# Kernel tuning notes

Hardware: AMD Instinct MI355X
Metric: run time of the kernel (lower is better)

Reference implementation:

```python
import jax, jax.numpy as jnp
import numpy as np

B, S, DIN, DOUT = 2, 4096, 4096, 11008

def setup_inputs() -> dict:
    key = jax.random.key(0)
    k1, k2, k3 = jax.random.split(key, 3)
    x = jax.random.normal(k1, (B, S, DIN), dtype=jnp.float32)
    # kaiming-uniform-ish full-precision weight
    bound_w = 1.0 / np.sqrt(DIN)
    weight = jax.random.uniform(k2, (DOUT, DIN), dtype=jnp.float32, minval=-bound_w, maxval=bound_w)
    bias = jax.random.uniform(k3, (DOUT,), dtype=jnp.float32, minval=-bound_w, maxval=bound_w)
    return {"x": x, "weight": weight, "bias": bias}

def reference(x, weight, bias):
    # Binarize weight to {-1, 0, +1} via sign (matches torch.sign), scale by mean |w| (detached)
    binary_w = jnp.sign(weight)                                  # [DOUT, DIN]
    scale = jax.lax.stop_gradient(jnp.mean(jnp.abs(weight)))    # scalar
    w_q = binary_w * scale
    # F.linear: x @ w_q.T + bias
    out = jnp.einsum('bsi,oi->bso', x, w_q) + bias               # [B, S, DOUT]
    return out
```

## Files before the change

kernel.cpp:

```cpp
#include <hip/hip_runtime.h>

#define MDIM 8192
#define KDIM 4096
#define NDIM 11008

#define NBLK_W 1024

typedef float f32x4 __attribute__((ext_vector_type(4)));
typedef int   i32x4 __attribute__((ext_vector_type(4)));
typedef char  c4    __attribute__((ext_vector_type(4)));

#define GAS __attribute__((address_space(1)))
#define LAS __attribute__((address_space(3)))

__global__ __launch_bounds__(256) void k_convert_w(const float* __restrict__ w,
                                                   char* __restrict__ wq,
                                                   float* __restrict__ partials) {
  const int n4 = (NDIM * KDIM) / 4;
  const int stride = gridDim.x * blockDim.x;
  float s = 0.f;
  for (int i = blockIdx.x * blockDim.x + threadIdx.x; i < n4; i += stride) {
    f32x4 v = ((const f32x4*)w)[i];
    s += fabsf(v.x) + fabsf(v.y) + fabsf(v.z) + fabsf(v.w);
    c4 q;
    q.x = v.x > 0.f ? 1 : (v.x < 0.f ? -1 : 0);
    q.y = v.y > 0.f ? 1 : (v.y < 0.f ? -1 : 0);
    q.z = v.z > 0.f ? 1 : (v.z < 0.f ? -1 : 0);
    q.w = v.w > 0.f ? 1 : (v.w < 0.f ? -1 : 0);
    ((c4*)wq)[i] = q;
  }
  #pragma unroll
  for (int off = 32; off > 0; off >>= 1) s += __shfl_down(s, off, 64);
  __shared__ float red[4];
  if ((threadIdx.x & 63) == 0) red[threadIdx.x >> 6] = s;
  __syncthreads();
  if (threadIdx.x == 0) partials[blockIdx.x] = red[0] + red[1] + red[2] + red[3];
}

__global__ __launch_bounds__(256) void k_scale(const float* __restrict__ partials,
                                               float* __restrict__ scale) {
  float s = 0.f;
  for (int i = threadIdx.x; i < NBLK_W; i += 256) s += partials[i];
  #pragma unroll
  for (int off = 32; off > 0; off >>= 1) s += __shfl_down(s, off, 64);
  __shared__ float red[4];
  if ((threadIdx.x & 63) == 0) red[threadIdx.x >> 6] = s;
  __syncthreads();
  if (threadIdx.x == 0)
    *scale = (red[0] + red[1] + red[2] + red[3]) / (float)((size_t)NDIM * KDIM);
}

__global__ __launch_bounds__(256) void k_convert_x(const float* __restrict__ x,
                                                   char* __restrict__ xq,
                                                   float* __restrict__ sx) {
  const int row = blockIdx.x;
  const float* xr = x + (size_t)row * KDIM;
  const int t = (int)threadIdx.x;
  f32x4 v[4];
  float mx = 0.f;
  #pragma unroll
  for (int j = 0; j < 4; ++j) {
    v[j] = *(const f32x4*)(xr + j * 1024 + t * 4);
    mx = fmaxf(mx, fmaxf(fmaxf(fabsf(v[j].x), fabsf(v[j].y)),
                         fmaxf(fabsf(v[j].z), fabsf(v[j].w))));
  }
  #pragma unroll
  for (int off = 32; off > 0; off >>= 1) mx = fmaxf(mx, __shfl_xor(mx, off, 64));
  __shared__ float red[4];
  __shared__ float bmax;
  if ((t & 63) == 0) red[t >> 6] = mx;
  __syncthreads();
  if (t == 0) {
    float m2 = fmaxf(fmaxf(red[0], red[1]), fmaxf(red[2], red[3]));
    m2 = fmaxf(m2, 1e-20f);
    bmax = m2;
    sx[row] = m2 * (1.f / 127.f);
  }
  __syncthreads();
  const float r = 127.f / bmax;
  #pragma unroll
  for (int j = 0; j < 4; ++j) {
    int a = __float2int_rn(v[j].x * r), b = __float2int_rn(v[j].y * r);
    int c = __float2int_rn(v[j].z * r), d = __float2int_rn(v[j].w * r);
    a = a > 127 ? 127 : (a < -127 ? -127 : a);
    b = b > 127 ? 127 : (b < -127 ? -127 : b);
    c = c > 127 ? 127 : (c < -127 ? -127 : c);
    d = d > 127 ? 127 : (d < -127 ? -127 : d);
    c4 q; q.x = (char)a; q.y = (char)b; q.z = (char)c; q.w = (char)d;
    *(c4*)(xq + (size_t)row * KDIM + j * 1024 + t * 4) = q;
  }
}


#define BAR()  __builtin_amdgcn_s_barrier()
#define SB0()  __builtin_amdgcn_sched_barrier(0)
#define PRIO1() __builtin_amdgcn_s_setprio(1)
#define PRIO0() __builtin_amdgcn_s_setprio(0)
#define VM(N)  asm volatile("s_waitcnt vmcnt(" #N ")" ::: "memory")

#define STAGE(GP, GROWB, LDSBASE, KT) do {                                            \
  const char* _s = (GP) + (size_t)((GROWB) + srow) * KDIM + (KT)*64 + scol;           \
  char* _d = lds + (LDSBASE) + tid*16;                                                \
  __builtin_amdgcn_global_load_lds((const GAS unsigned int*)_s,                       \
                                   (LAS unsigned int*)_d, 16, 0, 0);                  \
} while (0)

#define LOAD_B2(DST, BUF, NH)                                                         \
  _Pragma("unroll") for (int ni = 0; ni < 2; ++ni)                                    \
    DST[ni] = *(const i32x4*)&lds[(BUF)*24576 + 8192 + bWOff + (NH)*2048 + ni*1024    \
                                  + rowoff + rcol];

#define LOAD_A2(DST, BUF, MH)                                                         \
  _Pragma("unroll") for (int mi = 0; mi < 2; ++mi)                                    \
    DST[mi] = *(const i32x4*)&lds[(BUF)*24576 + aWOff + (MH)*2048 + mi*1024           \
                                  + rowoff + rcol];

#define MFMA4(AF, MB, BQ, NB)                                                         \
  _Pragma("unroll") for (int mi = 0; mi < 2; ++mi)                                    \
  _Pragma("unroll") for (int ni = 0; ni < 2; ++ni)                                    \
    acc[(MB)+mi][(NB)+ni] = __builtin_amdgcn_mfma_i32_16x16x64_i8(                    \
        AF[mi], BQ[ni], acc[(MB)+mi][(NB)+ni], 0, 0, 0);

__global__ __launch_bounds__(512, 4) void k_gemm256(const char* __restrict__ A,
                                                    const char* __restrict__ B,
                                                    const float* __restrict__ bias,
                                                    const float* __restrict__ sx,
                                                    const float* __restrict__ scale_p,
                                                    float* __restrict__ C) {
  extern __shared__ char lds[];

  const int nTn = NDIM / 256;
  const int nwg = (MDIM / 128) * nTn;
  int wg = (int)blockIdx.x;
  wg = (wg & 7) * (nwg / 8) + (wg >> 3);
  const int band = wg / (nTn * 8);
  const int rem  = wg % (nTn * 8);
  const int tn   = rem >> 3;
  const int tm   = band * 8 + (rem & 7);

  const int tid  = (int)threadIdx.x;
  const int lane = tid & 63;
  const int wave = tid >> 6;
  const int wm   = wave >> 2;
  const int wn   = wave & 3;
  const int l15  = lane & 15;

  const int rowoff = l15 * 64;
  const int rcol = ((lane >> 4) << 4) ^ (((l15 >> 1) & 3) << 4);
  const int srow = tid >> 2;
  const int scol = ((tid & 3) << 4) ^ (((tid >> 3) & 3) << 4);

  const int aWOff = wm * 4096;
  const int bWOff = wn * 4096;
  const int aRow = tm * 128;
  const int bRow = tn * 256;

  i32x4 acc[4][4];
  #pragma unroll
  for (int i = 0; i < 4; ++i)
    #pragma unroll
    for (int j = 0; j < 4; ++j) acc[i][j] = i32x4{0, 0, 0, 0};

  i32x4 af[2], bq01[2], bq23[2];

  STAGE(A, aRow,        0,     0);
  STAGE(B, bRow,        8192,  0);
  STAGE(B, bRow + 128,  16384, 0);
  STAGE(A, aRow,        24576, 1);
  VM(0);
  SB0();
  BAR();
  LOAD_A2(af, 0, 0); LOAD_B2(bq01, 0, 0);

  #pragma unroll 1
  for (int i = 0; i < 32; ++i) {
    const int kA = 2 * i + 1;
    const int kB = (2 * i + 2 > 63) ? 63 : 2 * i + 2;
    const int kC = (2 * i + 3 > 63) ? 63 : 2 * i + 3;
    PRIO1(); MFMA4(af, 0, bq01, 0); PRIO0(); SB0();
    LOAD_B2(bq23, 0, 1);
    STAGE(B, bRow,       32768, kA);
    BAR();
    PRIO1(); MFMA4(af, 0, bq23, 2); PRIO0(); SB0();
    LOAD_A2(af, 0, 1);
    STAGE(B, bRow + 128, 40960, kA);
    BAR();
    PRIO1(); MFMA4(af, 2, bq01, 0); PRIO0(); SB0();
    VM(0); SB0();
    BAR();
    PRIO1(); MFMA4(af, 2, bq23, 2); PRIO0(); SB0();
    LOAD_A2(af, 1, 0); LOAD_B2(bq01, 1, 0);
    STAGE(A, aRow,       0,     kB);
    BAR();
    PRIO1(); MFMA4(af, 0, bq01, 0); PRIO0(); SB0();
    LOAD_B2(bq23, 1, 1);
    STAGE(B, bRow,       8192,  kB);
    BAR();
    PRIO1(); MFMA4(af, 0, bq23, 2); PRIO0(); SB0();
    LOAD_A2(af, 1, 1);
    STAGE(B, bRow + 128, 16384, kB);
    BAR();
    PRIO1(); MFMA4(af, 2, bq01, 0); PRIO0(); SB0();
    VM(0); SB0();
    BAR();
    PRIO1(); MFMA4(af, 2, bq23, 2); PRIO0(); SB0();
    LOAD_A2(af, 0, 0); LOAD_B2(bq01, 0, 0);
    STAGE(A, aRow,       24576, kC);
    BAR();
  }

  VM(0);

  const float sc = *scale_p;
  float bv[4];
  #pragma unroll
  for (int ni = 0; ni < 4; ++ni) bv[ni] = bias[tn * 256 + wn * 64 + ni * 16 + l15];

  #pragma unroll
  for (int mi = 0; mi < 4; ++mi) {
    #pragma unroll
    for (int r = 0; r < 4; ++r) {
      const int m = tm * 128 + wm * 64 + mi * 16 + (lane >> 4) * 4 + r;
      const float srow_scale = sc * sx[m];
      float* crow = C + (size_t)m * NDIM + tn * 256 + wn * 64;
      #pragma unroll
      for (int ni = 0; ni < 4; ++ni)
        crow[ni * 16 + l15] = srow_scale * (float)acc[mi][ni][r] + bv[ni];
    }
  }
}

extern "C" void kernel_launch(void* const* d_in, const int* in_sizes, int n_in,
                              void* d_out, int out_size, void* d_ws, size_t ws_size,
                              hipStream_t stream) {
  const float* x = (const float*)d_in[0];
  const float* w = (const float*)d_in[1];
  const float* bias = (const float*)d_in[2];
  float* out = (float*)d_out;

  char* ws = (char*)d_ws;
  const size_t XQ_BYTES = (size_t)MDIM * KDIM;
  const size_t WQ_BYTES = (size_t)NDIM * KDIM;
  char* xq = ws;
  char* wq = ws + XQ_BYTES;
  float* sx = (float*)(ws + XQ_BYTES + WQ_BYTES);
  float* partials = sx + MDIM;
  float* scale = partials + NBLK_W;

  k_convert_w<<<NBLK_W, 256, 0, stream>>>(w, wq, partials);
  k_scale<<<1, 256, 0, stream>>>(partials, scale);
  k_convert_x<<<MDIM, 256, 0, stream>>>(x, xq, sx);

  (void)hipFuncSetAttribute((const void*)k_gemm256,
                            hipFuncAttributeMaxDynamicSharedMemorySize, 49152);
  const int grid = (MDIM / 128) * (NDIM / 256);
  k_gemm256<<<grid, 512, 49152, stream>>>(xq, wq, bias, sx, scale, out);
}
```

Measured before the change: 517.7 us.

## Triple-buffer LDS tiles with rotating buffers and partial vmcnt waits

Result: faster. 503.1 us (-2.8%).

```diff
diff --git a/kernel.cpp b/kernel.cpp
--- a/kernel.cpp
+++ b/kernel.cpp
@@ -98,21 +98,21 @@
 #define PRIO0() __builtin_amdgcn_s_setprio(0)
 #define VM(N)  asm volatile("s_waitcnt vmcnt(" #N ")" ::: "memory")
 
-#define STAGE(GP, GROWB, LDSBASE, KT) do {                                            \
+#define STAGE(GP, GROWB, LDSOFF, KT) do {                                             \
   const char* _s = (GP) + (size_t)((GROWB) + srow) * KDIM + (KT)*64 + scol;           \
-  char* _d = lds + (LDSBASE) + tid*16;                                                \
+  char* _d = lds + (LDSOFF) + tid*16;                                                 \
   __builtin_amdgcn_global_load_lds((const GAS unsigned int*)_s,                       \
                                    (LAS unsigned int*)_d, 16, 0, 0);                  \
 } while (0)
 
-#define LOAD_B2(DST, BUF, NH)                                                         \
+#define LOAD_B2(DST, BASE, NH)                                                        \
   _Pragma("unroll") for (int ni = 0; ni < 2; ++ni)                                    \
-    DST[ni] = *(const i32x4*)&lds[(BUF)*24576 + 8192 + bWOff + (NH)*2048 + ni*1024    \
+    DST[ni] = *(const i32x4*)&lds[(BASE) + 8192 + bWOff + (NH)*2048 + ni*1024         \
                                   + rowoff + rcol];
 
-#define LOAD_A2(DST, BUF, MH)                                                         \
+#define LOAD_A2(DST, BASE, MH)                                                        \
   _Pragma("unroll") for (int mi = 0; mi < 2; ++mi)                                    \
-    DST[mi] = *(const i32x4*)&lds[(BUF)*24576 + aWOff + (MH)*2048 + mi*1024           \
+    DST[mi] = *(const i32x4*)&lds[(BASE) + aWOff + (MH)*2048 + mi*1024                \
                                   + rowoff + rcol];
 
 #define MFMA4(AF, MB, BQ, NB)                                                         \
@@ -163,50 +163,38 @@
 
   i32x4 af[2], bq01[2], bq23[2];
 
-  STAGE(A, aRow,        0,     0);
-  STAGE(B, bRow,        8192,  0);
-  STAGE(B, bRow + 128,  16384, 0);
-  STAGE(A, aRow,        24576, 1);
-  VM(0);
+  int b_c = 0, b_n = 24576, b_s = 49152;
+
+  STAGE(A, aRow,       0,             0);
+  STAGE(B, bRow,       8192,          0);
+  STAGE(B, bRow + 128, 16384,         0);
+  STAGE(A, aRow,       24576,         1);
+  STAGE(B, bRow,       24576 + 8192,  1);
+  STAGE(B, bRow + 128, 24576 + 16384, 1);
+  VM(3);
   SB0();
   BAR();
   LOAD_A2(af, 0, 0); LOAD_B2(bq01, 0, 0);
 
   #pragma unroll 1
-  for (int i = 0; i < 32; ++i) {
-    const int kA = 2 * i + 1;
-    const int kB = (2 * i + 2 > 63) ? 63 : 2 * i + 2;
-    const int kC = (2 * i + 3 > 63) ? 63 : 2 * i + 3;
+  for (int i = 0; i < 64; ++i) {
+    const int kS = (i + 2 > 63) ? 63 : i + 2;
     PRIO1(); MFMA4(af, 0, bq01, 0); PRIO0(); SB0();
-    LOAD_B2(bq23, 0, 1);
-    STAGE(B, bRow,       32768, kA);
+    LOAD_B2(bq23, b_c, 1);
+    STAGE(A, aRow, b_s, kS);
     BAR();
     PRIO1(); MFMA4(af, 0, bq23, 2); PRIO0(); SB0();
-    LOAD_A2(af, 0, 1);
-    STAGE(B, bRow + 128, 40960, kA);
+    LOAD_A2(af, b_c, 1);
+    STAGE(B, bRow, b_s + 8192, kS);
     BAR();
     PRIO1(); MFMA4(af, 2, bq01, 0); PRIO0(); SB0();
-    VM(0); SB0();
+    STAGE(B, bRow + 128, b_s + 16384, kS);
+    VM(3); SB0();
     BAR();
     PRIO1(); MFMA4(af, 2, bq23, 2); PRIO0(); SB0();
-    LOAD_A2(af, 1, 0); LOAD_B2(bq01, 1, 0);
-    STAGE(A, aRow,       0,     kB);
-    BAR();
-    PRIO1(); MFMA4(af, 0, bq01, 0); PRIO0(); SB0();
-    LOAD_B2(bq23, 1, 1);
-    STAGE(B, bRow,       8192,  kB);
-    BAR();
-    PRIO1(); MFMA4(af, 0, bq23, 2); PRIO0(); SB0();
-    LOAD_A2(af, 1, 1);
-    STAGE(B, bRow + 128, 16384, kB);
-    BAR();
-    PRIO1(); MFMA4(af, 2, bq01, 0); PRIO0(); SB0();
-    VM(0); SB0();
-    BAR();
-    PRIO1(); MFMA4(af, 2, bq23, 2); PRIO0(); SB0();
-    LOAD_A2(af, 0, 0); LOAD_B2(bq01, 0, 0);
-    STAGE(A, aRow,       24576, kC);
-    BAR();
+    LOAD_A2(af, b_n, 0); LOAD_B2(bq01, b_n, 0);
+    BAR();
+    const int t = b_c; b_c = b_n; b_n = b_s; b_s = t;
   }
 
   VM(0);
@@ -252,7 +240,7 @@
   k_convert_x<<<MDIM, 256, 0, stream>>>(x, xq, sx);
 
   (void)hipFuncSetAttribute((const void*)k_gemm256,
-                            hipFuncAttributeMaxDynamicSharedMemorySize, 49152);
+                            hipFuncAttributeMaxDynamicSharedMemorySize, 73728);
   const int grid = (MDIM / 128) * (NDIM / 256);
-  k_gemm256<<<grid, 512, 49152, stream>>>(xq, wq, bias, sx, scale, out);
-}
+  k_gemm256<<<grid, 512, 73728, stream>>>(xq, wq, bias, sx, scale, out);
+}
```
